# Performance work log

Measured on AMD Instinct MI355X. Metric: run time of the kernel, lower is better.

Reference implementation:

```python
import jax, jax.numpy as jnp
import numpy as np

C = 256
EPS = 1e-5


def setup_inputs() -> dict:
    key = jax.random.key(0)
    ks = jax.random.split(key, 10)
    B, H, W = 4, 64, 64
    x1 = jax.random.normal(ks[0], (B, C, H, W), dtype=jnp.float32)
    x2 = jax.random.normal(ks[1], (B, C, H, W), dtype=jnp.float32)
    s = 1.0 / np.sqrt(C)
    qw = jax.random.normal(ks[2], (C, C), dtype=jnp.float32) * s
    qb = jax.random.normal(ks[3], (C,), dtype=jnp.float32) * 0.01
    kw = jax.random.normal(ks[4], (C, C), dtype=jnp.float32) * s
    kb = jax.random.normal(ks[5], (C,), dtype=jnp.float32) * 0.01
    vw = jax.random.normal(ks[6], (C, C), dtype=jnp.float32) * s
    vb = jax.random.normal(ks[7], (C,), dtype=jnp.float32) * 0.01
    ln_w = jnp.ones((C,), dtype=jnp.float32)
    ln_b = jnp.zeros((C,), dtype=jnp.float32)
    return {"x1": x1, "x2": x2, "qw": qw, "qb": qb, "kw": kw, "kb": kb,
            "vw": vw, "vb": vb, "ln_w": ln_w, "ln_b": ln_b}


def _conv1x1(x, w, b):
    # 1x1 conv == per-pixel matmul over channels. x: [B,C,H,W], w: [O,C]
    return jnp.einsum('oc,bchw->bohw', w, x) + b[None, :, None, None]


def reference(x1, x2, qw, qb, kw, kb, vw, vb, ln_w, ln_b):
    q = _conv1x1(x1, qw, qb)   # [B,C,H,W]
    k = _conv1x1(x2, kw, kb)   # [B,C,H,W]
    v = _conv1x1(x2, vw, vb)   # [B,C,H,W]
    # scores: [B,H,W,I,J]; softmax over LAST axis (j) only, as in the torch code
    scores = jnp.einsum('bchw,bcij->bhwij', q, k)
    attn = jax.nn.softmax(scores, axis=-1)
    fusion = jnp.einsum('bhwij,bcij->bchw', attn, v)  # [B,C,H,W]
    # LayerNorm2d: normalize over channel dim per spatial location
    mean = jnp.mean(fusion, axis=1, keepdims=True)
    var = jnp.var(fusion, axis=1, keepdims=True)
    normed = (fusion - mean) * jax.lax.rsqrt(var + EPS)
    return normed * ln_w[None, :, None, None] + ln_b[None, :, None, None]
```

## Files before the change

### kernel.cpp

```cpp
#include <hip/hip_runtime.h>


#define CDIM 256
#define NPOS 4096
#define BATCH 4
#define EPSV 1e-5f

typedef _Float16 f16;
typedef __attribute__((ext_vector_type(4))) _Float16 f16x4;
typedef __attribute__((ext_vector_type(8))) _Float16 f16x8;
typedef __attribute__((ext_vector_type(4))) float f32x4;
typedef __attribute__((ext_vector_type(16))) float f32x16;

#define WST       264
#define V_STRIDE  72
#define DQ_STRIDE 72
#define F_STRIDE  68

#define LBAR() asm volatile("s_waitcnt lgkmcnt(0)\n\ts_barrier" ::: "memory")


static __device__ __forceinline__ f16x8 cvt8(const float* __restrict__ p) {
    float4 w0 = *(const float4*)p;
    float4 w1 = *(const float4*)(p + 4);
    f16x8 r;
    r[0] = (f16)w0.x; r[1] = (f16)w0.y; r[2] = (f16)w0.z; r[3] = (f16)w0.w;
    r[4] = (f16)w1.x; r[5] = (f16)w1.y; r[6] = (f16)w1.z; r[7] = (f16)w1.w;
    return r;
}

__global__ __launch_bounds__(256, 4) void prep_kernel(
    const float* __restrict__ x1, const float* __restrict__ x2,
    const float* __restrict__ qw, const float* __restrict__ kw,
    const float* __restrict__ vw,
    f16* __restrict__ X1T, f16* __restrict__ X2T, f16* __restrict__ W16)
{
    const int id = blockIdx.x;
    const int t  = threadIdx.x;
    if (id < 2048) {
        __shared__ f16 T[64 * 72];
        const float* xs = (id & 1) ? x2 : x1;
        f16* dst        = (id & 1) ? X2T : X1T;
        const int t2 = id >> 1;
        const int b  = t2 >> 8;
        const int rm = t2 & 255;
        const int c0 = (rm >> 6) * 64;
        const int n0 = (rm & 63) * 64;
        const float* src = xs + ((size_t)b * CDIM + c0) * NPOS + n0;
        const int rr = t >> 6, col = t & 63;
        #pragma unroll
        for (int j = 0; j < 16; ++j) {
            int row = rr + j * 4;
            T[col * 72 + row] = (f16)src[(size_t)row * NPOS + col];
        }
        __syncthreads();
        const int n = t >> 3, lc = (t & 7) * 8;
        f16* d0 = dst + ((size_t)b * NPOS + n0) * CDIM + c0;
        #pragma unroll
        for (int j = 0; j < 2; ++j) {
            int nn = n + j * 32;
            *(f16x8*)(d0 + (size_t)nn * CDIM + lc) = *(const f16x8*)&T[nn * 72 + lc];
        }
    } else {
        const int wblk = id - 2048;
        const int pr = wblk >> 2, h = wblk & 3;
        const float* W = (pr == 0 ? qw : pr == 1 ? kw : vw) + (size_t)h * 64 * CDIM;
        f16* D = W16 + (size_t)pr * CDIM * CDIM + (size_t)h * 64 * CDIM;
        #pragma unroll
        for (int i = 0; i < 8; ++i) {
            int g = t + i * 256;
            int row = g >> 5, col = (g & 31) * 8;
            *(f16x8*)(D + (size_t)row * CDIM + col) = cvt8(W + (size_t)row * CDIM + col);
        }
    }
}

__global__ __launch_bounds__(256, 2) void gemm_kernel(
    const f16* __restrict__ X1T, const f16* __restrict__ X2T,
    const f16* __restrict__ W16,
    const float* __restrict__ qb, const float* __restrict__ kb,
    const float* __restrict__ vb,
    f16* __restrict__ Qg, f16* __restrict__ Kf, f16* __restrict__ Vf)
{
    __shared__ f16 Xs[64 * WST];
    __shared__ f16 Wh[64 * WST];
    __shared__ f16 Ds[64 * DQ_STRIDE];
    __shared__ float biasS[256];

    const int id = blockIdx.x;
    const int pr  = id >> 8;
    const int rem = id & 255;
    const int b   = rem >> 6;
    const int p0  = (rem & 63) << 6;
    const f16* XT = (pr == 0) ? X1T : X2T;
    const f16* Wp = W16 + (size_t)pr * CDIM * CDIM;
    const float* bias = pr == 0 ? qb : pr == 1 ? kb : vb;

    const int t = threadIdx.x, w = t >> 6, l = t & 63, lm = l & 31, lh = l >> 5;
    const int pt = w & 1, ot = w >> 1;

    biasS[t] = bias[t];
    #pragma unroll
    for (int it = 0; it < 8; ++it) {
        int p = w * 16 + it * 2 + lh;
        *(f16x8*)&Xs[p * WST + lm * 8] =
            *(const f16x8*)(XT + ((size_t)(b * NPOS + p0 + p)) * CDIM + lm * 8);
    }

    for (int q = 0; q < 4; ++q) {
        #pragma unroll
        for (int i = 0; i < 8; ++i) {
            int g = t + i * 256;
            int row = g >> 5, col = (g & 31) * 8;
            *(f16x8*)&Wh[row * WST + col] =
                *(const f16x8*)(Wp + (size_t)(q * 64 + row) * CDIM + col);
        }
        __syncthreads();

        f32x16 accA = {}, accB = {};
        #pragma unroll
        for (int ks = 0; ks < 16; ks += 2) {
            f16x8 x0 = *(const f16x8*)&Xs[(pt * 32 + lm) * WST + ks * 16 + lh * 8];
            f16x8 w0 = *(const f16x8*)&Wh[(ot * 32 + lm) * WST + ks * 16 + lh * 8];
            f16x8 x1v = *(const f16x8*)&Xs[(pt * 32 + lm) * WST + (ks + 1) * 16 + lh * 8];
            f16x8 w1 = *(const f16x8*)&Wh[(ot * 32 + lm) * WST + (ks + 1) * 16 + lh * 8];
            if (pr < 2) {
                accA = __builtin_amdgcn_mfma_f32_32x32x16_f16(x0, w0, accA, 0, 0, 0);
                accB = __builtin_amdgcn_mfma_f32_32x32x16_f16(x1v, w1, accB, 0, 0, 0);
            } else {
                accA = __builtin_amdgcn_mfma_f32_32x32x16_f16(w0, x0, accA, 0, 0, 0);
                accB = __builtin_amdgcn_mfma_f32_32x32x16_f16(w1, x1v, accB, 0, 0, 0);
            }
        }

        if (pr < 2) {
            int o_l = ot * 32 + lm;
            float bv = biasS[q * 64 + o_l];
            #pragma unroll
            for (int r = 0; r < 16; ++r) {
                int p_l = pt * 32 + (r & 3) + 8 * (r >> 2) + 4 * lh;
                Ds[p_l * DQ_STRIDE + o_l] = (f16)(accA[r] + accB[r] + bv);
            }
        } else {
            #pragma unroll
            for (int r = 0; r < 16; ++r) {
                int o_l = ot * 32 + (r & 3) + 8 * (r >> 2) + 4 * lh;
                Ds[o_l * DQ_STRIDE + pt * 32 + lm] =
                    (f16)(accA[r] + accB[r] + biasS[q * 64 + o_l]);
            }
        }
        __syncthreads();

        if (pr == 0) {
            #pragma unroll
            for (int j = 0; j < 2; ++j) {
                int row = (t >> 3) + j * 32;
                int cc  = (t & 7) * 8;
                f16x8 vdat = *(const f16x8*)&Ds[row * DQ_STRIDE + cc];
                *(f16x8*)(Qg + ((size_t)(b * NPOS + p0 + row)) * CDIM + q * 64 + cc) = vdat;
            }
        } else if (pr == 1) {
            #pragma unroll
            for (int i = 0; i < 2; ++i) {
                int idx  = t + i * 256;
                int kt_l = idx >> 8;
                int ks_l = (idx >> 6) & 3;
                int l2   = idx & 63;
                f16x8 vdat = *(const f16x8*)&Ds[(kt_l * 32 + (l2 & 31)) * DQ_STRIDE +
                                                ks_l * 16 + (l2 >> 5) * 8];
                size_t fo = (((size_t)b * 128 + (p0 >> 5) + kt_l) * 16 + q * 4 + ks_l) * 512
                            + l2 * 8;
                *(f16x8*)(Kf + fo) = vdat;
            }
        } else {
            #pragma unroll
            for (int i = 0; i < 2; ++i) {
                int idx  = t + i * 256;
                int ct_l = idx >> 8;
                int kb_  = (idx >> 6) & 3;
                int l2   = idx & 63;
                f16x8 vdat = *(const f16x8*)&Ds[(ct_l * 32 + (l2 & 31)) * DQ_STRIDE +
                                                kb_ * 16 + (l2 >> 5) * 8];
                size_t fo = ((((size_t)b * 64 + (p0 >> 6)) * 8 + q * 2 + ct_l) * 4 + kb_) * 512
                            + l2 * 8;
                *(f16x8*)(Vf + fo) = vdat;
            }
        }
        __syncthreads();
    }
}

__global__ __launch_bounds__(256, 2) void attn_kernel(
    const f16* __restrict__ Qg, const f16* __restrict__ Kf, const f16* __restrict__ Vf,
    float* __restrict__ Fp)
{
    __shared__ f16   Pl[2][64 * V_STRIDE];
    __shared__ float RedM[2][2][64], RedS[2][2][64];

    const int t    = threadIdx.x;
    const int L    = (int)((blockIdx.x & 7) * 64 + (blockIdx.x >> 3));
    const int grp  = L >> 6;
    const int b    = grp >> 1;
    const int half = grp & 1;
    const int qt   = L & 63;
    const int p0   = qt << 6;
    const int bq   = b * 64 + qt;
    const int w    = t >> 6;
    const int l    = t & 63;
    const int lm   = l & 31;
    const int lh   = l >> 5;
    const int spt  = w & 1;
    const int skt  = w >> 1;

    f16x8 qf[16];
    {
        const f16* qptr = Qg + (size_t)(b * NPOS + p0 + spt * 32 + lm) * CDIM + lh * 8;
        #pragma unroll
        for (int ks = 0; ks < 16; ++ks) qf[ks] = *(const f16x8*)(qptr + ks * 16);
    }

    const f16* Kfb = Kf + (size_t)b * 128 * 16 * 512;
    const f16* Vfb = Vf + (size_t)b * 64 * 8 * 4 * 512;

    f32x16 facc[4] = {};

    for (int it = 0; it < 32; ++it) {
        const int ch = half * 32 + it;
        const int pb = it & 1;

        const f16* Vt = Vfb + (size_t)ch * 8 * 4 * 512;
        f16x8 vf0[4], vf1[4];
        #pragma unroll
        for (int kb = 0; kb < 4; ++kb) {
            vf0[kb] = *(const f16x8*)(Vt + (size_t)((2 * w) * 4 + kb) * 512 + l * 8);
            vf1[kb] = *(const f16x8*)(Vt + (size_t)((2 * w + 1) * 4 + kb) * 512 + l * 8);
        }

        const f16* Kt = Kfb + (size_t)(ch * 2 + skt) * 16 * 512;
        f32x16 st = {};
        __builtin_amdgcn_s_setprio(1);
        #pragma unroll
        for (int ks = 0; ks < 16; ++ks) {
            f16x8 kf = *(const f16x8*)(Kt + (size_t)ks * 512 + l * 8);
            st = __builtin_amdgcn_mfma_f32_32x32x16_f16(kf, qf[ks], st, 0, 0, 0);
        }
        __builtin_amdgcn_s_setprio(0);

        float mx = st[0];
        #pragma unroll
        for (int r = 1; r < 16; ++r) mx = fmaxf(mx, st[r]);
        mx = fmaxf(mx, __shfl_xor(mx, 32));
        float ss = 0.f;
        #pragma unroll
        for (int r = 0; r < 16; ++r) {
            float e = __expf(st[r] - mx);
            st[r] = e;
            ss += e;
        }
        ss += __shfl_xor(ss, 32);
        if (lh == 0) { RedM[pb][skt][spt * 32 + lm] = mx; RedS[pb][skt][spt * 32 + lm] = ss; }
        LBAR();

        float mo = RedM[pb][skt ^ 1][spt * 32 + lm];
        float so = RedS[pb][skt ^ 1][spt * 32 + lm];
        float M  = fmaxf(mx, mo);
        float S  = ss * __expf(mx - M) + so * __expf(mo - M);
        float scale = __expf(mx - M) * __builtin_amdgcn_rcpf(S);

        #pragma unroll
        for (int rq = 0; rq < 4; ++rq) {
            f16x4 pk;
            #pragma unroll
            for (int q2 = 0; q2 < 4; ++q2) pk[q2] = (f16)(st[rq * 4 + q2] * scale);
            *(f16x4*)&Pl[pb][(spt * 32 + lm) * V_STRIDE + skt * 32 + rq * 8 + lh * 4] = pk;
        }
        LBAR();

        __builtin_amdgcn_s_setprio(1);
        #pragma unroll
        for (int kb = 0; kb < 4; ++kb) {
            f16x8 pf0 = *(const f16x8*)&Pl[pb][lm * V_STRIDE + kb * 16 + lh * 8];
            f16x8 pf1 = *(const f16x8*)&Pl[pb][(32 + lm) * V_STRIDE + kb * 16 + lh * 8];
            facc[0] = __builtin_amdgcn_mfma_f32_32x32x16_f16(vf0[kb], pf0, facc[0], 0, 0, 0);
            facc[1] = __builtin_amdgcn_mfma_f32_32x32x16_f16(vf0[kb], pf1, facc[1], 0, 0, 0);
            facc[2] = __builtin_amdgcn_mfma_f32_32x32x16_f16(vf1[kb], pf0, facc[2], 0, 0, 0);
            facc[3] = __builtin_amdgcn_mfma_f32_32x32x16_f16(vf1[kb], pf1, facc[3], 0, 0, 0);
        }
        __builtin_amdgcn_s_setprio(0);
    }

    float* dst = Fp + ((size_t)bq * 2 + half) * (CDIM * 64);
    #pragma unroll
    for (int ii = 0; ii < 2; ++ii)
        #pragma unroll
        for (int jj = 0; jj < 2; ++jj)
            #pragma unroll
            for (int r = 0; r < 16; ++r) {
                int c = w * 64 + ii * 32 + (r & 3) + 8 * (r >> 2) + 4 * lh;
                int p = jj * 32 + lm;
                dst[c * 64 + p] = facc[ii * 2 + jj][r];
            }
}

__global__ __launch_bounds__(256, 2) void merge_ln_kernel(
    const float* __restrict__ Fp, const float* __restrict__ ln_w,
    const float* __restrict__ ln_b, float* __restrict__ out)
{
    __shared__ float Fs[256 * F_STRIDE];
    __shared__ float redS[16 * 64], redQ[16 * 64];
    __shared__ float lnw_s[256], lnb_s[256];
    __shared__ float mu_s[64], rs_s[64];

    const int t  = threadIdx.x;
    const int bq = blockIdx.x;
    const int b  = bq >> 6;
    const int p0 = (bq & 63) << 6;

    lnw_s[t] = ln_w[t]; lnb_s[t] = ln_b[t];

    const int pb = (t & 15) * 4;
    const int cg = t >> 4;
    const float* base = Fp + (size_t)bq * 2 * (CDIM * 64);

    f32x4 s4 = {}, q4 = {};
    #pragma unroll 4
    for (int ci = 0; ci < 16; ++ci) {
        int c = cg * 16 + ci;
        size_t off = (size_t)c * 64 + pb;
        f32x4 v = *(const f32x4*)(base + off);
        v += *(const f32x4*)(base + (size_t)(CDIM * 64) + off);
        *(f32x4*)&Fs[c * F_STRIDE + pb] = v;
        s4 += v; q4 += v * v;
    }
    #pragma unroll
    for (int k2 = 0; k2 < 4; ++k2) {
        redS[cg * 64 + pb + k2] = s4[k2];
        redQ[cg * 64 + pb + k2] = q4[k2];
    }
    __syncthreads();
    if (t < 64) {
        float ss = 0.f, qq = 0.f;
        #pragma unroll
        for (int g2 = 0; g2 < 16; ++g2) { ss += redS[g2 * 64 + t]; qq += redQ[g2 * 64 + t]; }
        float mean = ss * (1.0f / 256.0f);
        float var  = qq * (1.0f / 256.0f) - mean * mean;
        mu_s[t] = mean;
        rs_s[t] = rsqrtf(var + EPSV);
    }
    __syncthreads();
    const int p   = t & 63;
    const int cg2 = t >> 6;
    const float mu = mu_s[p], rs = rs_s[p];
    float* dst = out + (size_t)b * CDIM * NPOS + p0 + p;
    #pragma unroll 4
    for (int ci = 0; ci < 64; ++ci) {
        int c = cg2 * 64 + ci;
        dst[(size_t)c * NPOS] = (Fs[c * F_STRIDE + p] - mu) * rs * lnw_s[c] + lnb_s[c];
    }
}

extern "C" void kernel_launch(void* const* d_in, const int* in_sizes, int n_in,
                              void* d_out, int out_size, void* d_ws, size_t ws_size,
                              hipStream_t stream)
{
    const float* x1  = (const float*)d_in[0];
    const float* x2  = (const float*)d_in[1];
    const float* qw  = (const float*)d_in[2];
    const float* qb  = (const float*)d_in[3];
    const float* kw  = (const float*)d_in[4];
    const float* kb  = (const float*)d_in[5];
    const float* vw  = (const float*)d_in[6];
    const float* vb  = (const float*)d_in[7];
    const float* lnw = (const float*)d_in[8];
    const float* lnb = (const float*)d_in[9];

    const size_t tsz = (size_t)BATCH * NPOS * CDIM;
    f16* Qg  = (f16*)d_ws;
    f16* Kf  = Qg + tsz;
    f16* Vf  = Kf + tsz;
    f16* X1T = Vf + tsz;
    f16* X2T = X1T + tsz;
    f16* W16 = X2T + tsz;
    float* Fp = (float*)X1T;

    prep_kernel<<<2060, 256, 0, stream>>>(x1, x2, qw, kw, vw, X1T, X2T, W16);
    gemm_kernel<<<768, 256, 0, stream>>>(X1T, X2T, W16, qb, kb, vb, Qg, Kf, Vf);
    attn_kernel<<<512, 256, 0, stream>>>(Qg, Kf, Vf, Fp);
    merge_ln_kernel<<<256, 256, 0, stream>>>(Fp, lnw, lnb, (float*)d_out);
}
```

Before: 231.5 us.

## Split attention key range three ways and raise attention occupancy to three blocks

The attention kernel now splits the 64 key chunks into three partitions (22/21/21) instead of two. That gives 768 blocks, and launch bounds allow three blocks per CU. V fragment loads move from the top of each iteration into the PV loop, which cuts register pressure so the higher occupancy can fit. The merge/LayerNorm kernel now sums three partial outputs. The trade-off is more partial-sum memory and more global traffic in the merge, and V load latency is now less hidden behind the QK MFMAs.

```diff
diff --git a/kernel.cpp b/kernel.cpp
--- a/kernel.cpp
+++ b/kernel.cpp
@@ -190,7 +190,7 @@
     }
 }
 
-__global__ __launch_bounds__(256, 2) void attn_kernel(
+__global__ __launch_bounds__(256, 3) void attn_kernel(
     const f16* __restrict__ Qg, const f16* __restrict__ Kf, const f16* __restrict__ Vf,
     float* __restrict__ Fp)
 {
@@ -198,13 +198,13 @@
     __shared__ float RedM[2][2][64], RedS[2][2][64];
 
     const int t    = threadIdx.x;
-    const int L    = (int)((blockIdx.x & 7) * 64 + (blockIdx.x >> 3));
-    const int grp  = L >> 6;
-    const int b    = grp >> 1;
-    const int half = grp & 1;
-    const int qt   = L & 63;
-    const int p0   = qt << 6;
-    const int bq   = b * 64 + qt;
+    const int L    = (int)((blockIdx.x & 7) * 96 + (blockIdx.x >> 3));
+    const int bq   = L & 255;
+    const int tau  = L >> 8;
+    const int b    = bq >> 6;
+    const int p0   = (bq & 63) << 6;
+    const int c0   = (tau == 0) ? 0 : 22 + (tau - 1) * 21;
+    const int cnt  = (tau == 0) ? 22 : 21;
     const int w    = t >> 6;
     const int l    = t & 63;
     const int lm   = l & 31;
@@ -224,17 +224,9 @@
 
     f32x16 facc[4] = {};
 
-    for (int it = 0; it < 32; ++it) {
-        const int ch = half * 32 + it;
+    for (int it = 0; it < cnt; ++it) {
+        const int ch = c0 + it;
         const int pb = it & 1;
-
-        const f16* Vt = Vfb + (size_t)ch * 8 * 4 * 512;
-        f16x8 vf0[4], vf1[4];
-        #pragma unroll
-        for (int kb = 0; kb < 4; ++kb) {
-            vf0[kb] = *(const f16x8*)(Vt + (size_t)((2 * w) * 4 + kb) * 512 + l * 8);
-            vf1[kb] = *(const f16x8*)(Vt + (size_t)((2 * w + 1) * 4 + kb) * 512 + l * 8);
-        }
 
         const f16* Kt = Kfb + (size_t)(ch * 2 + skt) * 16 * 512;
         f32x16 st = {};
@@ -276,20 +268,23 @@
         }
         LBAR();
 
+        const f16* Vt = Vfb + (size_t)ch * 8 * 4 * 512;
         __builtin_amdgcn_s_setprio(1);
         #pragma unroll
         for (int kb = 0; kb < 4; ++kb) {
+            f16x8 vf0 = *(const f16x8*)(Vt + (size_t)((2 * w) * 4 + kb) * 512 + l * 8);
+            f16x8 vf1 = *(const f16x8*)(Vt + (size_t)((2 * w + 1) * 4 + kb) * 512 + l * 8);
             f16x8 pf0 = *(const f16x8*)&Pl[pb][lm * V_STRIDE + kb * 16 + lh * 8];
             f16x8 pf1 = *(const f16x8*)&Pl[pb][(32 + lm) * V_STRIDE + kb * 16 + lh * 8];
-            facc[0] = __builtin_amdgcn_mfma_f32_32x32x16_f16(vf0[kb], pf0, facc[0], 0, 0, 0);
-            facc[1] = __builtin_amdgcn_mfma_f32_32x32x16_f16(vf0[kb], pf1, facc[1], 0, 0, 0);
-            facc[2] = __builtin_amdgcn_mfma_f32_32x32x16_f16(vf1[kb], pf0, facc[2], 0, 0, 0);
-            facc[3] = __builtin_amdgcn_mfma_f32_32x32x16_f16(vf1[kb], pf1, facc[3], 0, 0, 0);
+            facc[0] = __builtin_amdgcn_mfma_f32_32x32x16_f16(vf0, pf0, facc[0], 0, 0, 0);
+            facc[1] = __builtin_amdgcn_mfma_f32_32x32x16_f16(vf0, pf1, facc[1], 0, 0, 0);
+            facc[2] = __builtin_amdgcn_mfma_f32_32x32x16_f16(vf1, pf0, facc[2], 0, 0, 0);
+            facc[3] = __builtin_amdgcn_mfma_f32_32x32x16_f16(vf1, pf1, facc[3], 0, 0, 0);
         }
         __builtin_amdgcn_s_setprio(0);
     }
 
-    float* dst = Fp + ((size_t)bq * 2 + half) * (CDIM * 64);
+    float* dst = Fp + ((size_t)bq * 3 + tau) * (CDIM * 64);
     #pragma unroll
     for (int ii = 0; ii < 2; ++ii)
         #pragma unroll
@@ -320,7 +315,7 @@
 
     const int pb = (t & 15) * 4;
     const int cg = t >> 4;
-    const float* base = Fp + (size_t)bq * 2 * (CDIM * 64);
+    const float* base = Fp + (size_t)bq * 3 * (CDIM * 64);
 
     f32x4 s4 = {}, q4 = {};
     #pragma unroll 4
@@ -329,6 +324,7 @@
         size_t off = (size_t)c * 64 + pb;
         f32x4 v = *(const f32x4*)(base + off);
         v += *(const f32x4*)(base + (size_t)(CDIM * 64) + off);
+        v += *(const f32x4*)(base + (size_t)(2 * CDIM * 64) + off);
         *(f32x4*)&Fs[c * F_STRIDE + pb] = v;
         s4 += v; q4 += v * v;
     }
@@ -385,6 +381,6 @@
 
     prep_kernel<<<2060, 256, 0, stream>>>(x1, x2, qw, kw, vw, X1T, X2T, W16);
     gemm_kernel<<<768, 256, 0, stream>>>(X1T, X2T, W16, qb, kb, vb, Qg, Kf, Vf);
-    attn_kernel<<<512, 256, 0, stream>>>(Qg, Kf, Vf, Fp);
+    attn_kernel<<<768, 256, 0, stream>>>(Qg, Kf, Vf, Fp);
     merge_ln_kernel<<<256, 256, 0, stream>>>(Fp, lnw, lnb, (float*)d_out);
 }
```

Measured after the change: 287.0 us. 24.0% more time.
